# Performance work log

Hardware: AMD Instinct MI355X
Metric: run time of the kernel (lower is better)

The kernel has to match this reference:

```python
import jax, jax.numpy as jnp
import numpy as np

IN_FEATURES = 4096
OUT_FEATURES = 11008
TOKENS = 32


def ternarize_weight(w):
    # abs-mean scale, clamped; threshold at 0.7*abs_mean
    abs_mean = jnp.maximum(jnp.mean(jnp.abs(w)), 1e-5)
    threshold = 0.7 * abs_mean
    q = jnp.where(w > threshold, 1.0, jnp.where(w < -threshold, -1.0, 0.0))
    # straight-through estimator: forward value q*abs_mean, grad passes to w
    return w + jax.lax.stop_gradient(q * abs_mean - w)


def setup_inputs() -> dict:
    key = jax.random.key(0)
    kx, kw = jax.random.split(key)
    x = jax.random.normal(kx, (TOKENS, IN_FEATURES), dtype=jnp.float32)
    # master fp32 weights, init std = 1/sqrt(in_features) as in the module
    weight = jax.random.normal(kw, (OUT_FEATURES, IN_FEATURES), dtype=jnp.float32) / np.sqrt(IN_FEATURES)
    return {"x": x, "weight": weight}


def reference(x, weight):
    # ternary_active=True, ternary_alpha=1.0 path: fully ternarized weights
    w_q = ternarize_weight(weight)
    # F.linear(x, w): [T, in] @ [out, in]^T -> [T, out]
    return jnp.einsum('ti,oi->to', x, w_q)
```

## Files before the change

kernel.cpp:

```cpp
#include <hip/hip_runtime.h>
#include <hip/hip_bf16.h>
#include <stdint.h>

#define IN_F 4096
#define OUT_F 11008
#define TOKENS 32
#define NELEM_W (OUT_F * IN_F)

typedef __attribute__((ext_vector_type(8))) __bf16 bf16x8;
typedef __attribute__((ext_vector_type(4))) float  f32x4;

__device__ __forceinline__ uint32_t bfr(float v) {
    uint32_t u = __float_as_uint(v);
    uint32_t r = u + 0x7FFFu + ((u >> 16) & 1u);
    return r >> 16;
}

#define ABSUM_BLOCKS 2048
#define XCVT_BLOCKS  64

__global__ __launch_bounds__(256) void absum_xcvt_kernel(const float* __restrict__ w,
                                                         const float* __restrict__ x,
                                                         double* __restrict__ ws_sum,
                                                         uint4* __restrict__ xb) {
    if (blockIdx.x >= ABSUM_BLOCKS) {
        int i = (blockIdx.x - ABSUM_BLOCKS) * 256 + threadIdx.x;
        const float4* x4 = (const float4*)x;
        float4 a0 = x4[i * 2];
        float4 a1 = x4[i * 2 + 1];
        uint4 o;
        o.x = bfr(a0.x) | (bfr(a0.y) << 16);
        o.y = bfr(a0.z) | (bfr(a0.w) << 16);
        o.z = bfr(a1.x) | (bfr(a1.y) << 16);
        o.w = bfr(a1.z) | (bfr(a1.w) << 16);
        xb[i] = o;
        return;
    }
    int tid = blockIdx.x * blockDim.x + threadIdx.x;
    int stride = ABSUM_BLOCKS * 256;
    const float4* w4 = (const float4*)w;
    const int n4 = NELEM_W / 4;
    float s = 0.f;
    for (int i = tid; i < n4; i += stride) {
        float4 v = w4[i];
        s += fabsf(v.x) + fabsf(v.y) + fabsf(v.z) + fabsf(v.w);
    }
    for (int off = 32; off > 0; off >>= 1)
        s += __shfl_down(s, off, 64);
    __shared__ float wsum[4];
    int lane = threadIdx.x & 63;
    int wv   = threadIdx.x >> 6;
    if (lane == 0) wsum[wv] = s;
    __syncthreads();
    if (threadIdx.x == 0) {
        float t = wsum[0] + wsum[1] + wsum[2] + wsum[3];
        atomicAdd(ws_sum, (double)t);
    }
}

__global__ void finalize_kernel(double* __restrict__ ws) {
    double mean = ws[0] / (double)NELEM_W;
    if (mean < 1e-5) mean = 1e-5;
    float mf = (float)mean;
    float* f = (float*)ws;
    f[2] = 0.7f * mf;
    f[3] = mf;
}

__device__ __forceinline__ uint32_t tern1(float v, float thr) {
    uint32_t u  = __float_as_uint(v);
    uint32_t pm = (u & 0x80000000u) | 0x3F800000u;
    return (__builtin_fabsf(v) > thr) ? pm : 0u;
}

__device__ __forceinline__ bf16x8 tern8(float4 b0, float4 b1, float thr) {
    uint32_t q0 = tern1(b0.x, thr), q1 = tern1(b0.y, thr);
    uint32_t q2 = tern1(b0.z, thr), q3 = tern1(b0.w, thr);
    uint32_t q4 = tern1(b1.x, thr), q5 = tern1(b1.y, thr);
    uint32_t q6 = tern1(b1.z, thr), q7 = tern1(b1.w, thr);
    union { uint32_t u[4]; bf16x8 v; } U;
    U.u[0] = (q0 >> 16) | (q1 & 0xFFFF0000u);
    U.u[1] = (q2 >> 16) | (q3 & 0xFFFF0000u);
    U.u[2] = (q4 >> 16) | (q5 & 0xFFFF0000u);
    U.u[3] = (q6 >> 16) | (q7 & 0xFFFF0000u);
    return U.v;
}

#define CHUNKS 8
#define WAVE_LDS 2304
#define SMEM_BYTES 9216

__global__ __launch_bounds__(256, 4) void ternary_gemm(const float* __restrict__ w,
                                                       const float* __restrict__ wsf,
                                                       const __bf16* __restrict__ xb,
                                                       float* __restrict__ out) {
    __shared__ char smem_raw[SMEM_BYTES];
    const float thr   = wsf[2];
    const float scale = wsf[3];
    const int og   = blockIdx.x >> 1;
    const int kh   = blockIdx.x & 1;
    const int tid  = threadIdx.x;
    const int wv   = tid >> 6;
    const int lane = tid & 63;
    const int col  = lane & 15;
    const int quad = lane >> 4;
    const int srow = lane >> 2;
    const int scol = lane & 3;

    const int kbase = kh * 2048 + wv * 512;

    const float* wp = w + (size_t)(og * 16 + srow) * IN_F + kbase + scol * 16;
    char* stage = smem_raw + wv * WAVE_LDS;
    char* wr0   = stage + srow * 144 + scol * 32;
    const char* rd = stage + col * 144;
    const __bf16* xp = xb + (size_t)col * IN_F + kbase + quad * 8;

    f32x4 acc0 = {0.f, 0.f, 0.f, 0.f};
    f32x4 acc1 = {0.f, 0.f, 0.f, 0.f};

    float4 f0 = ((const float4*)wp)[0];
    float4 f1 = ((const float4*)wp)[1];
    float4 f2 = ((const float4*)wp)[2];
    float4 f3 = ((const float4*)wp)[3];

    for (int c = 0; c < CHUNKS; ++c) {
        bf16x8 t0 = tern8(f0, f1, thr);
        bf16x8 t1 = tern8(f2, f3, thr);
        *(bf16x8*)(wr0)      = t0;
        *(bf16x8*)(wr0 + 16) = t1;

        if (c + 1 < CHUNKS) {
            const float4* np = (const float4*)(wp + (c + 1) * 64);
            f0 = np[0]; f1 = np[1]; f2 = np[2]; f3 = np[3];
        }

#pragma unroll
        for (int s = 0; s < 2; ++s) {
            bf16x8 bw = *(const bf16x8*)(rd + (s * 4 + quad) * 16);
            bf16x8 a0 = *(const bf16x8*)(xp + c * 64 + s * 32);
            bf16x8 a1 = *(const bf16x8*)(xp + c * 64 + s * 32 + 16 * IN_F);
            acc0 = __builtin_amdgcn_mfma_f32_16x16x32_bf16(a0, bw, acc0, 0, 0, 0);
            acc1 = __builtin_amdgcn_mfma_f32_16x16x32_bf16(a1, bw, acc1, 0, 0, 0);
        }
    }

    __syncthreads();
    float* red  = (float*)smem_raw;
    float* base = red + wv * 512;
#pragma unroll
    for (int r = 0; r < 4; ++r) base[r * 64 + lane]       = acc0[r];
#pragma unroll
    for (int r = 0; r < 4; ++r) base[256 + r * 64 + lane] = acc1[r];
    __syncthreads();

#pragma unroll
    for (int p = tid; p < 512; p += 256) {
        int t = p >> 4, cc = p & 15;
        int a = t >> 4;
        int q = (t >> 2) & 3;
        int r = t & 3;
        int idx = a * 256 + r * 64 + q * 16 + cc;
        float s = red[idx] + red[512 + idx] + red[1024 + idx] + red[1536 + idx];
        atomicAdd(out + (size_t)t * OUT_F + og * 16 + cc, s * scale);
    }
}

extern "C" void kernel_launch(void* const* d_in, const int* in_sizes, int n_in,
                              void* d_out, int out_size, void* d_ws, size_t ws_size,
                              hipStream_t stream) {
    const float* x = (const float*)d_in[0];
    const float* w = (const float*)d_in[1];
    float* out     = (float*)d_out;
    double* wsd    = (double*)d_ws;
    uint4* xb      = (uint4*)((char*)d_ws + 64);

    hipMemsetAsync(d_ws, 0, 16, stream);
    hipMemsetAsync(d_out, 0, sizeof(float) * TOKENS * OUT_F, stream);

    absum_xcvt_kernel<<<ABSUM_BLOCKS + XCVT_BLOCKS, 256, 0, stream>>>(w, x, wsd, xb);
    finalize_kernel<<<1, 1, 0, stream>>>(wsd);
    ternary_gemm<<<(OUT_F / 16) * 2, 256, 0, stream>>>(w, (const float*)d_ws,
                                                       (const __bf16*)((char*)d_ws + 64), out);
}
```

Baseline: 300.8 us.

## Coalesce weight loads across lanes and prefetch x fragments one chunk ahead

Reassigns weight loading so the 16 lanes of each quad read consecutive float4s of one row, giving fully coalesced 256-byte row segments instead of 64-byte per-lane strips. The LDS staging writes are split into four 8-byte stores to match. The bf16 activation fragments are now also loaded one chunk ahead and double-buffered in registers. Launch bounds drop to 3 blocks per SM and the loop is unrolled by 2, which trades occupancy for more registers.

```diff
diff --git a/kernel.cpp b/kernel.cpp
--- a/kernel.cpp
+++ b/kernel.cpp
@@ -73,24 +73,20 @@
     return (__builtin_fabsf(v) > thr) ? pm : 0u;
 }
 
-__device__ __forceinline__ bf16x8 tern8(float4 b0, float4 b1, float thr) {
-    uint32_t q0 = tern1(b0.x, thr), q1 = tern1(b0.y, thr);
-    uint32_t q2 = tern1(b0.z, thr), q3 = tern1(b0.w, thr);
-    uint32_t q4 = tern1(b1.x, thr), q5 = tern1(b1.y, thr);
-    uint32_t q6 = tern1(b1.z, thr), q7 = tern1(b1.w, thr);
-    union { uint32_t u[4]; bf16x8 v; } U;
-    U.u[0] = (q0 >> 16) | (q1 & 0xFFFF0000u);
-    U.u[1] = (q2 >> 16) | (q3 & 0xFFFF0000u);
-    U.u[2] = (q4 >> 16) | (q5 & 0xFFFF0000u);
-    U.u[3] = (q6 >> 16) | (q7 & 0xFFFF0000u);
-    return U.v;
+__device__ __forceinline__ uint2 tern4(float4 b, float thr) {
+    uint32_t q0 = tern1(b.x, thr), q1 = tern1(b.y, thr);
+    uint32_t q2 = tern1(b.z, thr), q3 = tern1(b.w, thr);
+    uint2 r;
+    r.x = (q0 >> 16) | (q1 & 0xFFFF0000u);
+    r.y = (q2 >> 16) | (q3 & 0xFFFF0000u);
+    return r;
 }
 
 #define CHUNKS 8
 #define WAVE_LDS 2304
 #define SMEM_BYTES 9216
 
-__global__ __launch_bounds__(256, 4) void ternary_gemm(const float* __restrict__ w,
+__global__ __launch_bounds__(256, 3) void ternary_gemm(const float* __restrict__ w,
                                                        const float* __restrict__ wsf,
                                                        const __bf16* __restrict__ xb,
                                                        float* __restrict__ out) {
@@ -104,44 +100,61 @@
     const int lane = tid & 63;
     const int col  = lane & 15;
     const int quad = lane >> 4;
-    const int srow = lane >> 2;
-    const int scol = lane & 3;
+    const int rlan = lane & 15;
 
-    const int kbase = kh * 2048 + wv * 512;
+    const int kw = kh * 2048 + wv * 512;
 
-    const float* wp = w + (size_t)(og * 16 + srow) * IN_F + kbase + scol * 16;
+    const float* wp = w + (size_t)(og * 16 + quad) * IN_F + kw + rlan * 4;
     char* stage = smem_raw + wv * WAVE_LDS;
-    char* wr0   = stage + srow * 144 + scol * 32;
+    char* wr    = stage + quad * 144 + rlan * 8;
     const char* rd = stage + col * 144;
-    const __bf16* xp = xb + (size_t)col * IN_F + kbase + quad * 8;
+    const __bf16* xq = xb + (size_t)col * IN_F + kw + quad * 8;
 
     f32x4 acc0 = {0.f, 0.f, 0.f, 0.f};
     f32x4 acc1 = {0.f, 0.f, 0.f, 0.f};
 
-    float4 f0 = ((const float4*)wp)[0];
-    float4 f1 = ((const float4*)wp)[1];
-    float4 f2 = ((const float4*)wp)[2];
-    float4 f3 = ((const float4*)wp)[3];
+    float4 w0 = *(const float4*)(wp);
+    float4 w1 = *(const float4*)(wp + 4 * IN_F);
+    float4 w2 = *(const float4*)(wp + 8 * IN_F);
+    float4 w3 = *(const float4*)(wp + 12 * IN_F);
+    bf16x8 a00 = *(const bf16x8*)(xq);
+    bf16x8 a01 = *(const bf16x8*)(xq + 32);
+    bf16x8 a10 = *(const bf16x8*)(xq + 16 * IN_F);
+    bf16x8 a11 = *(const bf16x8*)(xq + 16 * IN_F + 32);
 
+#pragma unroll 2
     for (int c = 0; c < CHUNKS; ++c) {
-        bf16x8 t0 = tern8(f0, f1, thr);
-        bf16x8 t1 = tern8(f2, f3, thr);
-        *(bf16x8*)(wr0)      = t0;
-        *(bf16x8*)(wr0 + 16) = t1;
+        uint2 t0 = tern4(w0, thr);
+        uint2 t1 = tern4(w1, thr);
+        uint2 t2 = tern4(w2, thr);
+        uint2 t3 = tern4(w3, thr);
+        *(uint2*)(wr)        = t0;
+        *(uint2*)(wr + 576)  = t1;
+        *(uint2*)(wr + 1152) = t2;
+        *(uint2*)(wr + 1728) = t3;
 
+        bf16x8 n00 = a00, n01 = a01, n10 = a10, n11 = a11;
         if (c + 1 < CHUNKS) {
-            const float4* np = (const float4*)(wp + (c + 1) * 64);
-            f0 = np[0]; f1 = np[1]; f2 = np[2]; f3 = np[3];
+            const float*  np = wp + (c + 1) * 64;
+            const __bf16* xn = xq + (c + 1) * 64;
+            w0  = *(const float4*)(np);
+            w1  = *(const float4*)(np + 4 * IN_F);
+            w2  = *(const float4*)(np + 8 * IN_F);
+            w3  = *(const float4*)(np + 12 * IN_F);
+            n00 = *(const bf16x8*)(xn);
+            n01 = *(const bf16x8*)(xn + 32);
+            n10 = *(const bf16x8*)(xn + 16 * IN_F);
+            n11 = *(const bf16x8*)(xn + 16 * IN_F + 32);
         }
 
-#pragma unroll
-        for (int s = 0; s < 2; ++s) {
-            bf16x8 bw = *(const bf16x8*)(rd + (s * 4 + quad) * 16);
-            bf16x8 a0 = *(const bf16x8*)(xp + c * 64 + s * 32);
-            bf16x8 a1 = *(const bf16x8*)(xp + c * 64 + s * 32 + 16 * IN_F);
-            acc0 = __builtin_amdgcn_mfma_f32_16x16x32_bf16(a0, bw, acc0, 0, 0, 0);
-            acc1 = __builtin_amdgcn_mfma_f32_16x16x32_bf16(a1, bw, acc1, 0, 0, 0);
-        }
+        bf16x8 bw0 = *(const bf16x8*)(rd + quad * 16);
+        bf16x8 bw1 = *(const bf16x8*)(rd + 64 + quad * 16);
+        acc0 = __builtin_amdgcn_mfma_f32_16x16x32_bf16(a00, bw0, acc0, 0, 0, 0);
+        acc1 = __builtin_amdgcn_mfma_f32_16x16x32_bf16(a10, bw0, acc1, 0, 0, 0);
+        acc0 = __builtin_amdgcn_mfma_f32_16x16x32_bf16(a01, bw1, acc0, 0, 0, 0);
+        acc1 = __builtin_amdgcn_mfma_f32_16x16x32_bf16(a11, bw1, acc1, 0, 0, 0);
+
+        a00 = n00; a01 = n01; a10 = n10; a11 = n11;
     }
 
     __syncthreads();
```

After: 293.0 us. 2.6% less time.
